# Optimization experiments

Measured on AMD Instinct MI355X. Metric: run time of the kernel, lower is better.

Reference implementation:

```python
import jax, jax.numpy as jnp
import numpy as np

N = 100000   # nodes
E = 1600000  # edges
W = 12       # window_size / timesteps
CIN, CMID, COUT, K, DIL = 16, 32, 32, 3, 1


def setup_inputs() -> dict:
    key = jax.random.key(0)
    k = jax.random.split(key, 6)
    x = jax.random.normal(k[0], (W, N, CIN), dtype=jnp.float32)
    A = jax.random.randint(k[1], (2, E), 0, N, dtype=jnp.int32)
    ew = jax.random.uniform(k[2], (E,), dtype=jnp.float32)  # positive edge weights
    gcn_w = jax.random.normal(k[3], (W, CIN, CMID), dtype=jnp.float32) * (1.0 / np.sqrt(CIN))
    gcn_b = jnp.zeros((W, CMID), dtype=jnp.float32)
    conv_w = jax.random.normal(k[4], (COUT, CMID, K), dtype=jnp.float32) * (1.0 / np.sqrt(CMID * K))
    conv_b = jnp.zeros((COUT,), dtype=jnp.float32)
    return {"x": x, "A": A, "ew": ew, "gcn_w": gcn_w, "gcn_b": gcn_b,
            "conv_w": conv_w, "conv_b": conv_b}


def reference(x, A, ew, gcn_w, gcn_b, conv_w, conv_b):
    row, col = A[0], A[1]  # src, dst
    # GCN normalization (add_self_loops=False): deg over dst with edge weights
    deg = jax.ops.segment_sum(ew, col, num_segments=N)
    dis = jnp.where(deg > 0, jax.lax.rsqrt(jnp.where(deg > 0, deg, 1.0)), 0.0)
    norm = dis[row] * ew * dis[col]  # [E]

    # one GCNConv per timestep, shared edge structure; scan keeps peak memory low
    def step(carry, inp):
        Wt, bt, xt = inp
        h = xt @ Wt                                    # [N, CMID]
        msg = h[row] * norm[:, None]                   # gather + scale, [E, CMID]
        agg = jax.ops.segment_sum(msg, col, num_segments=N)  # scatter-add
        return carry, agg + bt

    _, outs = jax.lax.scan(step, None, (gcn_w, gcn_b, x))  # [W, N, CMID]

    # stack(dim=1) + transpose(1,2) -> [N, CMID, W], then temporal Conv1d ('same')
    y = jnp.transpose(outs, (1, 2, 0))
    pad = (K // 2) * DIL
    y = jax.lax.conv_general_dilated(
        y, conv_w, window_strides=(1,), padding=[(pad, pad)],
        rhs_dilation=(DIL,), dimension_numbers=("NCH", "OIH", "NCH"))
    y = y + conv_b[None, :, None]
    y = jnp.transpose(y, (0, 2, 1))  # [N, W, COUT]
    y = jnp.where(y >= 0, y, 0.01 * y)  # LeakyReLU; dropout p=0 is identity
    return y  # equivalent to the list [y[:, i, :] for i in range(W)]
```

## Files before the change

kernel.cpp:

```cpp
#include <hip/hip_runtime.h>

#define NN 100000
#define NE 1600000
#define WT 12
#define CI 16
#define CM 32
#define CO 32

#define FXS 33554432.0f

__device__ __forceinline__ unsigned bf16pack(float a, float b) {
    unsigned ua = __float_as_uint(a);
    unsigned ub = __float_as_uint(b);
    ua = (ua + 0x7FFFu + ((ua >> 16) & 1u)) >> 16;
    ub = (ub + 0x7FFFu + ((ub >> 16) & 1u)) >> 16;
    return ua | (ub << 16);
}

__global__ void k_xpose(const float* __restrict__ x, unsigned* __restrict__ xTb) {
    int f = blockIdx.x * 256 + threadIdx.x;
    if (f >= NN * 96) return;
    int n = f / 96;
    int u = f - n * 96;
    int t = u >> 3;
    int p = u & 7;
    const float2* x2 = (const float2*)x;
    float2 v = x2[((size_t)t * NN + n) * 8 + p];
    xTb[f] = bf16pack(v.x, v.y);
}

__global__ void k_count(const int* __restrict__ A, const float* __restrict__ ew,
                        unsigned long long* __restrict__ pk, int* __restrict__ rank) {
    int e = blockIdx.x * 256 + threadIdx.x;
    if (e >= NE) return;
    int c = A[NE + e];
    unsigned long long fx = (unsigned long long)(ew[e] * FXS + 0.5f);
    unsigned long long old = atomicAdd(&pk[c], (1ull << 40) | fx);
    rank[e] = (int)(old >> 40);
}

__global__ void k_dis_alloc(const unsigned long long* __restrict__ pk,
                            float* __restrict__ dis, int2* __restrict__ ds,
                            int* __restrict__ total) {
    int n = blockIdx.x * 256 + threadIdx.x;
    bool valid = (n < NN);
    int c = 0;
    if (valid) {
        unsigned long long v = pk[n];
        c = (int)(v >> 40);
        float d = (float)(v & ((1ull << 40) - 1)) * (1.0f / FXS);
        dis[n] = d > 0.0f ? rsqrtf(d) : 0.0f;
    }
    int lane = threadIdx.x & 63;
    int inc = c;
    #pragma unroll
    for (int o = 1; o < 64; o <<= 1) {
        int v = __shfl_up(inc, o, 64);
        if (lane >= o) inc += v;
    }
    int base = 0;
    if (lane == 63) base = atomicAdd(total, inc);
    base = __shfl(base, 63, 64);
    if (valid) ds[n] = make_int2(base + inc - c, c);
}

__global__ void k_scatter(const int* __restrict__ A, const float* __restrict__ ew,
                          const float* __restrict__ dis, const int2* __restrict__ ds,
                          const int* __restrict__ rank, float2* __restrict__ meta) {
    int e = blockIdx.x * 256 + threadIdx.x;
    if (e >= NE) return;
    int r = A[e];
    int c = A[NE + e];
    float w = dis[r] * ew[e];
    int p = ds[c].x + rank[e];
    meta[p] = make_float2(__int_as_float(r), w);
}

__global__ __launch_bounds__(256) void k_agg(const unsigned* __restrict__ xTb,
                      const int2* __restrict__ ds, const float* __restrict__ dis,
                      const float2* __restrict__ meta, float* __restrict__ xagg) {
    int wave = threadIdx.x >> 6;
    int lane = threadIdx.x & 63;
    int node = blockIdx.x * 4 + wave;
    int2 sc = ds[node];
    int s = __builtin_amdgcn_readfirstlane(sc.x);
    int c = __builtin_amdgcn_readfirstlane(sc.y);
    int li = lane < 48 ? lane : 47;
    float4 acc = make_float4(0.f, 0.f, 0.f, 0.f);
    const float2* mp = meta + s;
    #pragma unroll 4
    for (int i = 0; i < c; i++) {
        float2 m = mp[i];
        int src = __float_as_int(m.x);
        float w = m.y;
        uint2 u = ((const uint2*)(xTb + (size_t)src * 96))[li];
        acc.x += w * __uint_as_float(u.x << 16);
        acc.y += w * __uint_as_float(u.x & 0xFFFF0000u);
        acc.z += w * __uint_as_float(u.y << 16);
        acc.w += w * __uint_as_float(u.y & 0xFFFF0000u);
    }
    float dn = dis[node];
    acc.x *= dn; acc.y *= dn; acc.z *= dn; acc.w *= dn;
    if (lane < 48)
        ((float4*)(xagg + (size_t)node * 192))[lane] = acc;
}

__global__ void k_foldW(const float* __restrict__ gw, const float* __restrict__ cw,
                        float* __restrict__ M2) {
    int i = blockIdx.x * 256 + threadIdx.x;
    if (i >= WT * 3 * CI * CO) return;
    int co = i & 31;
    int rem = i >> 5;
    int ci = rem & 15;
    int kidx = rem % 48;
    int k = kidx >> 4;
    int t = rem / 48;
    int tp = t + k - 1;
    float s = 0.0f;
    if (tp >= 0 && tp < WT) {
        for (int cm = 0; cm < CM; cm++)
            s += gw[(tp * CI + ci) * CM + cm] * cw[co * (CM * 3) + cm * 3 + k];
    }
    M2[i] = s;
}

__global__ void k_foldB(const float* __restrict__ gb, const float* __restrict__ cw,
                        const float* __restrict__ cb, float* __restrict__ B2) {
    int i = blockIdx.x * 256 + threadIdx.x;
    if (i >= WT * CO) return;
    int co = i & 31;
    int t = i >> 5;
    float s = cb[co];
    for (int k = 0; k < 3; k++) {
        int tp = t + k - 1;
        if (tp < 0 || tp >= WT) continue;
        for (int cm = 0; cm < CM; cm++)
            s += gb[tp * CM + cm] * cw[co * (CM * 3) + cm * 3 + k];
    }
    B2[i] = s;
}

__global__ __launch_bounds__(256) void k_out(const float* __restrict__ xagg,
                                             const float* __restrict__ M2,
                                             const float* __restrict__ B2,
                                             float* __restrict__ out) {
    int wgid  = ((int)blockIdx.x & 7) * 588 + ((int)blockIdx.x >> 3);
    int chunk = wgid / 12;
    int t     = wgid - chunk * 12;
    int n     = chunk * 256 + (int)threadIdx.x;
    if (n >= NN) return;
    const float* xr = xagg + (size_t)n * 192;
    const float* Wt = M2 + (size_t)t * 48 * CO;
    float acc[CO];
    #pragma unroll
    for (int co = 0; co < CO; co++) acc[co] = B2[t * CO + co];
    #pragma unroll
    for (int k = 0; k < 3; k++) {
        int tp = t + k - 1;
        if (tp < 0 || tp >= WT) continue;
        const float4* xs = (const float4*)(xr + tp * 16);
        #pragma unroll
        for (int q = 0; q < 4; q++) {
            float4 v = xs[q];
            float vj[4] = {v.x, v.y, v.z, v.w};
            #pragma unroll
            for (int jj = 0; jj < 4; jj++) {
                float a = vj[jj];
                const float* wrow = Wt + ((k * 16 + q * 4 + jj) * CO);
                #pragma unroll
                for (int co = 0; co < CO; co++)
                    acc[co] += a * wrow[co];
            }
        }
    }
    float* o = out + ((size_t)n * WT + t) * CO;
    #pragma unroll
    for (int co = 0; co < CO; co += 4) {
        float4 v;
        v.x = acc[co]     >= 0.0f ? acc[co]     : 0.01f * acc[co];
        v.y = acc[co + 1] >= 0.0f ? acc[co + 1] : 0.01f * acc[co + 1];
        v.z = acc[co + 2] >= 0.0f ? acc[co + 2] : 0.01f * acc[co + 2];
        v.w = acc[co + 3] >= 0.0f ? acc[co + 3] : 0.01f * acc[co + 3];
        *(float4*)(o + co) = v;
    }
}

extern "C" void kernel_launch(void* const* d_in, const int* in_sizes, int n_in,
                              void* d_out, int out_size, void* d_ws, size_t ws_size,
                              hipStream_t stream) {
    const float* x  = (const float*)d_in[0];
    const int*   A  = (const int*)d_in[1];
    const float* ew = (const float*)d_in[2];
    const float* gw = (const float*)d_in[3];
    const float* gb = (const float*)d_in[4];
    const float* cw = (const float*)d_in[5];
    const float* cb = (const float*)d_in[6];
    float* out = (float*)d_out;
    float* ws  = (float*)d_ws;

    unsigned long long* pk = (unsigned long long*)ws;
    int*      total = (int*)(ws + 2 * NN);
    int*      rank  = (int*)(ws + 2 * NN + 32);
    float*    dis   = ws + 2 * NN + 32 + NE;
    int2*     ds    = (int2*)(ws + 3 * NN + 32 + NE);
    float2*   meta  = (float2*)(ws + 5 * NN + 32 + NE);
    unsigned* xTb   = (unsigned*)(ws + 5 * NN + 32 + 3 * NE);
    float*    M2    = ws + 5 * NN + 32 + 3 * NE + NN * 96;
    float*    B2    = M2 + WT * 3 * CI * CO;
    float*    xagg  = B2 + WT * CO;

    hipMemsetAsync(d_ws, 0, (size_t)(2 * NN + 32) * sizeof(float), stream);

    k_xpose    <<<(NN * 96) / 256, 256, 0, stream>>>(x, xTb);
    k_count    <<<(NE + 255) / 256, 256, 0, stream>>>(A, ew, pk, rank);
    k_dis_alloc<<<(NN + 255) / 256, 256, 0, stream>>>(pk, dis, ds, total);
    k_scatter  <<<(NE + 255) / 256, 256, 0, stream>>>(A, ew, dis, ds, rank, meta);
    k_agg      <<<NN / 4, 256, 0, stream>>>(xTb, ds, dis, meta, xagg);
    k_foldW    <<<(WT * 3 * CI * CO + 255) / 256, 256, 0, stream>>>(gw, cw, M2);
    k_foldB    <<<(WT * CO + 255) / 256, 256, 0, stream>>>(gb, cw, cb, B2);
    k_out      <<<4704, 256, 0, stream>>>(xagg, M2, B2, out);
}
```

Measured before the change: 555.3 us.

## Store aggregated features time-major and stage k_out inputs through LDS

```diff
diff --git a/kernel.cpp b/kernel.cpp
--- a/kernel.cpp
+++ b/kernel.cpp
@@ -6,6 +6,9 @@
 #define CI 16
 #define CM 32
 #define CO 32
+
+#define NCHUNK 392
+#define NND (NCHUNK * 256)
 
 #define FXS 33554432.0f
 
@@ -102,7 +105,7 @@
     float dn = dis[node];
     acc.x *= dn; acc.y *= dn; acc.z *= dn; acc.w *= dn;
     if (lane < 48)
-        ((float4*)(xagg + (size_t)node * 192))[lane] = acc;
+        ((float4*)xagg)[(size_t)(lane >> 2) * (NND * 4) + node * 4 + (lane & 3)] = acc;
 }
 
 __global__ void k_foldW(const float* __restrict__ gw, const float* __restrict__ cw,
@@ -147,41 +150,67 @@
     int wgid  = ((int)blockIdx.x & 7) * 588 + ((int)blockIdx.x >> 3);
     int chunk = wgid / 12;
     int t     = wgid - chunk * 12;
-    int n     = chunk * 256 + (int)threadIdx.x;
-    if (n >= NN) return;
-    const float* xr = xagg + (size_t)n * 192;
+    int tid   = (int)threadIdx.x;
+    int n     = chunk * 256 + tid;
+
+    __shared__ float lds[3 * 5120];
+
+    #pragma unroll
+    for (int p = 0; p < 3; p++) {
+        int tp = t + p - 1;
+        float* ldsp = lds + p * 5120;
+        if (tp >= 0 && tp < WT) {
+            const float4* gp = (const float4*)xagg + (size_t)tp * (NND * 4) + chunk * 1024;
+            #pragma unroll
+            for (int i = 0; i < 4; i++) {
+                int idx = i * 256 + tid;
+                float4 v = gp[idx];
+                *(float4*)(ldsp + (idx >> 2) * 20 + (idx & 3) * 4) = v;
+            }
+        } else {
+            #pragma unroll
+            for (int i = 0; i < 4; i++) {
+                int idx = i * 256 + tid;
+                *(float4*)(ldsp + (idx >> 2) * 20 + (idx & 3) * 4) =
+                    make_float4(0.f, 0.f, 0.f, 0.f);
+            }
+        }
+    }
+    __syncthreads();
+
     const float* Wt = M2 + (size_t)t * 48 * CO;
     float acc[CO];
     #pragma unroll
     for (int co = 0; co < CO; co++) acc[co] = B2[t * CO + co];
-    #pragma unroll
-    for (int k = 0; k < 3; k++) {
-        int tp = t + k - 1;
-        if (tp < 0 || tp >= WT) continue;
-        const float4* xs = (const float4*)(xr + tp * 16);
+
+    #pragma unroll
+    for (int p = 0; p < 3; p++) {
         #pragma unroll
         for (int q = 0; q < 4; q++) {
-            float4 v = xs[q];
+            float4 v = *(float4*)(lds + p * 5120 + tid * 20 + q * 4);
             float vj[4] = {v.x, v.y, v.z, v.w};
             #pragma unroll
             for (int jj = 0; jj < 4; jj++) {
                 float a = vj[jj];
-                const float* wrow = Wt + ((k * 16 + q * 4 + jj) * CO);
+                const float* wrow = Wt + ((p * 16 + q * 4 + jj) * CO);
                 #pragma unroll
                 for (int co = 0; co < CO; co++)
                     acc[co] += a * wrow[co];
             }
         }
     }
-    float* o = out + ((size_t)n * WT + t) * CO;
-    #pragma unroll
-    for (int co = 0; co < CO; co += 4) {
-        float4 v;
-        v.x = acc[co]     >= 0.0f ? acc[co]     : 0.01f * acc[co];
-        v.y = acc[co + 1] >= 0.0f ? acc[co + 1] : 0.01f * acc[co + 1];
-        v.z = acc[co + 2] >= 0.0f ? acc[co + 2] : 0.01f * acc[co + 2];
-        v.w = acc[co + 3] >= 0.0f ? acc[co + 3] : 0.01f * acc[co + 3];
-        *(float4*)(o + co) = v;
+
+    if (n < NN) {
+        float* o = out + ((size_t)n * WT + t) * CO;
+        #pragma unroll
+        for (int co = 0; co < CO; co += 4) {
+            float4 v;
+            v.x = acc[co]     >= 0.0f ? acc[co]     : 0.01f * acc[co];
+            v.y = acc[co + 1] >= 0.0f ? acc[co + 1] : 0.01f * acc[co + 1];
+            v.z = acc[co + 2] >= 0.0f ? acc[co + 2] : 0.01f * acc[co + 2];
+            v.w = acc[co + 3] >= 0.0f ? acc[co + 3] : 0.01f * acc[co + 3];
+            *(float4*)(o + co) = v;
+        }
     }
 }
 
@@ -218,5 +247,5 @@
     k_agg      <<<NN / 4, 256, 0, stream>>>(xTb, ds, dis, meta, xagg);
     k_foldW    <<<(WT * 3 * CI * CO + 255) / 256, 256, 0, stream>>>(gw, cw, M2);
     k_foldB    <<<(WT * CO + 255) / 256, 256, 0, stream>>>(gb, cw, cb, B2);
-    k_out      <<<4704, 256, 0, stream>>>(xagg, M2, B2, out);
-}
+    k_out      <<<12 * NCHUNK, 256, 0, stream>>>(xagg, M2, B2, out);
+}
```

Result: no change. 552.7 us (-0.5%).
